# Optimization experiments

Hardware: AMD Instinct MI355X
Metric: run time of the kernel (lower is better)

The kernel has to match this reference:

```python
import jax, jax.numpy as jnp
import numpy as np

B, S, D = 4, 2048, 2048
H, HD = 16, 128
ROPE_THETA = 10000.0


def rotate_half(x):
    half = x.shape[-1] // 2
    return jnp.concatenate([-x[..., half:], x[..., :half]], axis=-1)


def setup_inputs() -> dict:
    key = jax.random.key(0)
    ks = jax.random.split(key, 5)
    scale = 1.0 / np.sqrt(D)
    x = jax.random.normal(ks[0], (B, S, D), dtype=jnp.float32)
    wq = jax.random.normal(ks[1], (D, H * HD), dtype=jnp.float32) * scale
    wk = jax.random.normal(ks[2], (D, H * HD), dtype=jnp.float32) * scale
    wv = jax.random.normal(ks[3], (D, H * HD), dtype=jnp.float32) * scale
    wo = jax.random.normal(ks[4], (H * HD, D), dtype=jnp.float32) * scale
    # RoPE frequencies: freqs_cis real/imag parts, shape [S, HD//2]
    inv_freq = 1.0 / (ROPE_THETA ** (np.arange(0, HD, 2, dtype=np.float32) / HD))
    t = np.arange(S, dtype=np.float32)
    freqs = np.outer(t, inv_freq)  # [S, HD//2]
    cos = jnp.asarray(np.cos(freqs), dtype=jnp.float32)
    sin = jnp.asarray(np.sin(freqs), dtype=jnp.float32)
    return {"x": x, "wq": wq, "wk": wk, "wv": wv, "wo": wo, "cos": cos, "sin": sin}


def reference(x, wq, wk, wv, wo, cos, sin):
    batch, seq_len, _ = x.shape
    # QKV projections (no bias), reshape to [b, h, s, d]
    q = (x @ wq).reshape(batch, seq_len, H, HD).transpose(0, 2, 1, 3)
    k = (x @ wk).reshape(batch, seq_len, H, HD).transpose(0, 2, 1, 3)
    v = (x @ wv).reshape(batch, seq_len, H, HD)  # [b, s, h, d]
    # RoPE (half-split / rotate_half convention)
    cos_full = jnp.concatenate([cos, cos], axis=-1)[None, None, :seq_len, :]
    sin_full = jnp.concatenate([sin, sin], axis=-1)[None, None, :seq_len, :]
    q = q * cos_full + rotate_half(q) * sin_full
    k = k * cos_full + rotate_half(k) * sin_full
    # Scaled dot-product attention with causal mask
    logits = jnp.einsum('bhqd,bhkd->bhqk', q, k) / jnp.sqrt(jnp.float32(HD))
    causal = jnp.tril(jnp.ones((seq_len, seq_len), dtype=bool))
    logits = jnp.where(causal[None, None, :, :], logits, -1e10)
    weights = jax.nn.softmax(logits, axis=-1)
    out = jnp.einsum('bhqk,bkhd->bqhd', weights, v)
    out = out.reshape(batch, seq_len, H * HD)
    return out @ wo
```

## Files before the change

kernel.cpp:

```cpp
#include <hip/hip_runtime.h>
#include <cstdint>
#include <cstddef>

typedef unsigned short u16;
using bf16x8  = __attribute__((ext_vector_type(8))) short;
using floatx4 = __attribute__((ext_vector_type(4))) float;

__device__ __forceinline__ u16 f2bf(float f) {
    union { float f; unsigned u; } v; v.f = f;
    unsigned r = v.u + 0x7fffu + ((v.u >> 16) & 1u);
    return (u16)(r >> 16);
}
__device__ __forceinline__ float bf2f(u16 h) {
    union { unsigned u; float f; } v; v.u = ((unsigned)h) << 16; return v.f;
}
__device__ __forceinline__ floatx4 mfma16(bf16x8 a, bf16x8 b, floatx4 c) {
    return __builtin_amdgcn_mfma_f32_16x16x32_bf16(a, b, c, 0, 0, 0);
}
using gptr_t = const __attribute__((address_space(1))) unsigned int*;
using lptr_t = __attribute__((address_space(3))) unsigned int*;
__device__ __forceinline__ void lds16(const void* g, void* l) {
    __builtin_amdgcn_global_load_lds((gptr_t)g, (lptr_t)l, 16, 0, 0);
}
typedef __attribute__((address_space(3))) const u16* lds_cp;
__device__ __forceinline__ bf16x8 dsr128(const u16* p) {
    bf16x8 r;
    asm volatile("ds_read_b128 %0, %1" : "=v"(r) : "v"((lds_cp)p));
    return r;
}

#define ATT_SCALE 0.1275758218522532f

__global__ __launch_bounds__(256) void prep(const float* __restrict__ x,
                                            const float* __restrict__ wq, const float* __restrict__ wk,
                                            const float* __restrict__ wv, const float* __restrict__ wo,
                                            u16* __restrict__ xb,
                                            u16* __restrict__ wqkvb, u16* __restrict__ wob) {
    const int z = blockIdx.z;
    const int tx = threadIdx.x, ty = threadIdx.y;
    if (z < 4) {
        __shared__ float t[64][65];
        const float* in = (z == 0) ? wq : (z == 1) ? wk : (z == 2) ? wv : wo;
        u16* out = (z < 3) ? (wqkvb + (size_t)z * 2048 * 2048) : wob;
        int k0 = blockIdx.x * 64, n0 = blockIdx.y * 64;
#pragma unroll
        for (int i = 0; i < 16; ++i) {
            int r = i * 4 + ty;
            t[r][tx] = in[(size_t)(k0 + r) * 2048 + n0 + tx];
        }
        __syncthreads();
#pragma unroll
        for (int i = 0; i < 16; ++i) {
            int r = i * 4 + ty;
            out[(size_t)(n0 + r) * 2048 + k0 + tx] = f2bf(t[tx][r]);
        }
    } else {
        const int flat = ty * 64 + tx;
        const size_t base = (size_t)(blockIdx.y * 32 + blockIdx.x) * 256 + flat;
        const size_t stride = 1024 * 256;
#pragma unroll
        for (int it = 0; it < 16; ++it) {
            size_t i = (base + it * stride) * 4;
            float4 v = *(const float4*)&x[i];
            ushort4 r; r.x = f2bf(v.x); r.y = f2bf(v.y); r.z = f2bf(v.z); r.w = f2bf(v.w);
            *(ushort4*)&xb[i] = r;
        }
    }
}

template <int MODE>
__global__ __launch_bounds__(512, 2) void gemm_bt(const u16* __restrict__ A, const u16* __restrict__ B,
                                                  u16* __restrict__ Qo, u16* __restrict__ Ko, u16* __restrict__ Vt,
                                                  float* __restrict__ Co,
                                                  const float* __restrict__ cosb, const float* __restrict__ sinb) {
    __shared__ __align__(16) u16 sA[2][16384];
    __shared__ __align__(16) u16 sB[2][16384];

    const int nbx = (MODE == 0) ? 24 : 8;
    const int bid = blockIdx.x;
    const int q8 = (int)gridDim.x >> 3;
    const int wg = (bid & 7) * q8 + (bid >> 3);
    const int bx = wg % nbx, by = wg / nbx;
    const int m0 = by << 8, n0 = bx << 8;

    const int tid = threadIdx.x;
    const int w = tid >> 6, lane = tid & 63;
    const int wm = w >> 2, wn = w & 3;
    const int m16 = lane & 15, q4 = lane >> 4;
    const int lr = lane >> 3;
    const int lc8 = (lane & 7) ^ lr;
    const int wnbase = (wn >> 1) * 128 + (wn & 1) * 32;

    const u16* Ag = A + (size_t)(m0 + w * 16 + lr) * 2048 + lc8 * 8;
    const u16* Bg = B + (size_t)(n0 + w * 16 + lr) * 2048 + lc8 * 8;

    const int swz0 = ((q4 ^ (m16 & 7)) << 3);
    const int swz1 = (((4 + q4) ^ (m16 & 7)) << 3);

    floatx4 acc[8][4];
#pragma unroll
    for (int r = 0; r < 8; ++r)
#pragma unroll
        for (int c = 0; c < 4; ++c) acc[r][c] = (floatx4)0.0f;
    bf16x8 af[4][2];
    bf16x8 bf[4][2];

#define STAGE_A(b, h, t) do { \
    lds16(Ag + (size_t)((h) * 128) * 2048 + (t) * 64,     &sA[b][(h) * 8192 + w * 1024]);       \
    lds16(Ag + (size_t)((h) * 128 + 8) * 2048 + (t) * 64, &sA[b][(h) * 8192 + w * 1024 + 512]); \
} while (0)
#define STAGE_B(b, h, t) do { \
    lds16(Bg + (size_t)((h) * 128) * 2048 + (t) * 64,     &sB[b][(h) * 8192 + w * 1024]);       \
    lds16(Bg + (size_t)((h) * 128 + 8) * 2048 + (t) * 64, &sB[b][(h) * 8192 + w * 1024 + 512]); \
} while (0)
#define BAR() __builtin_amdgcn_s_barrier()
#define WAITL0() do { asm volatile("s_waitcnt lgkmcnt(0)" ::: "memory"); __builtin_amdgcn_sched_barrier(0); } while (0)
#define WAITL8() asm volatile("s_waitcnt lgkmcnt(8)" ::: "memory")
#define LDA_(cur, mq) do { _Pragma("unroll") for (int fr = 0; fr < 4; ++fr) { \
    const u16* p = &sA[cur][(wm * 128 + (mq) * 64 + fr * 16 + m16) * 64];      \
    af[fr][0] = dsr128(&p[swz0]);                                              \
    af[fr][1] = dsr128(&p[swz1]); } } while (0)
#define LDB_(cur, nq) do { _Pragma("unroll") for (int c = 0; c < 2; ++c) {     \
    const int j = (nq) * 2 + c;                                                \
    const u16* p = &sB[cur][(wnbase + (j & 1) * 16 + (j >> 1) * 64 + m16) * 64]; \
    bf[j][0] = dsr128(&p[swz0]);                                               \
    bf[j][1] = dsr128(&p[swz1]); } } while (0)
#define MM_(mq, nq) do { _Pragma("unroll") for (int kk = 0; kk < 2; ++kk)      \
    _Pragma("unroll") for (int fr = 0; fr < 4; ++fr)                           \
    _Pragma("unroll") for (int c = 0; c < 2; ++c)                              \
        acc[(mq) * 4 + fr][(nq) * 2 + c] =                                     \
            mfma16(af[fr][kk], bf[(nq) * 2 + c][kk], acc[(mq) * 4 + fr][(nq) * 2 + c]); } while (0)

    const int NT = 32;

    STAGE_B(0, 0, 0); STAGE_B(0, 1, 0);
    STAGE_A(0, 0, 0); STAGE_A(0, 1, 0);
    STAGE_B(1, 0, 1); STAGE_B(1, 1, 1);
    asm volatile("s_waitcnt vmcnt(4)" ::: "memory");
    __builtin_amdgcn_s_barrier();

#pragma unroll 2
    for (int t = 0; t < NT; ++t) {
        const int cur = t & 1;
        LDB_(cur, 0);
        LDA_(cur, 0);
        if (t + 1 < NT) STAGE_A(cur ^ 1, 0, t + 1);
        WAITL8();
        BAR();
        WAITL0();
        __builtin_amdgcn_s_setprio(1); MM_(0, 0); __builtin_amdgcn_s_setprio(0);
        BAR();
        LDB_(cur, 1);
        if (t + 1 < NT) STAGE_A(cur ^ 1, 1, t + 1);
        BAR();
        WAITL0();
        __builtin_amdgcn_s_setprio(1); MM_(0, 1); __builtin_amdgcn_s_setprio(0);
        BAR();
        LDA_(cur, 1);
        if (t + 2 < NT) STAGE_B(cur, 0, t + 2);
        BAR();
        WAITL0();
        __builtin_amdgcn_s_setprio(1); MM_(1, 1); __builtin_amdgcn_s_setprio(0);
        BAR();
        if (t + 2 < NT) STAGE_B(cur, 1, t + 2);
        BAR();
        __builtin_amdgcn_s_setprio(1); MM_(1, 0); __builtin_amdgcn_s_setprio(0);
        if (t + 2 < NT)      { asm volatile("s_waitcnt vmcnt(4)" ::: "memory"); }
        else if (t + 1 < NT) { asm volatile("s_waitcnt vmcnt(0)" ::: "memory"); }
        BAR();
    }

#undef STAGE_A
#undef STAGE_B
#undef BAR
#undef WAITL0
#undef WAITL8
#undef LDA_
#undef LDB_
#undef MM_

    if (MODE == 0) {
        const int which = n0 >> 11;
        if (which < 2) {
            u16* dst = (which == 0) ? Qo : Ko;
            const float sc = (which == 0) ? ATT_SCALE : 1.0f;
            const int h = ((n0 >> 7) + (wn >> 1)) & 15;
            const int dp0 = (wn & 1) * 32 + m16;
#pragma unroll
            for (int fr = 0; fr < 8; ++fr) {
                const int mb = m0 + wm * 128 + fr * 16 + q4 * 4;
#pragma unroll
                for (int c0 = 0; c0 < 2; ++c0) {
                    const int dp = dp0 + c0 * 16;
#pragma unroll
                    for (int i = 0; i < 4; ++i) {
                        const int mm = mb + i;
                        const int b = mm >> 11, s = mm & 2047;
                        const float cs = cosb[(size_t)s * 64 + dp];
                        const float sn = sinb[(size_t)s * 64 + dp];
                        const float lo = acc[fr][c0][i], hi = acc[fr][c0 + 2][i];
                        const size_t base = ((size_t)((b * 16 + h) * 2048 + s) << 7) + dp;
                        dst[base]      = f2bf((lo * cs - hi * sn) * sc);
                        dst[base + 64] = f2bf((hi * cs + lo * sn) * sc);
                    }
                }
            }
        } else {
#pragma unroll
            for (int fr = 0; fr < 8; ++fr) {
                const int mb = m0 + wm * 128 + fr * 16 + q4 * 4;
                const int b = mb >> 11, s = mb & 2047;
#pragma unroll
                for (int c = 0; c < 4; ++c) {
                    const int n = n0 + wnbase + (c & 1) * 16 + (c >> 1) * 64 + m16;
                    const int h = (n >> 7) & 15, d = n & 127;
                    ushort4 pk;
                    pk.x = f2bf(acc[fr][c][0]); pk.y = f2bf(acc[fr][c][1]);
                    pk.z = f2bf(acc[fr][c][2]); pk.w = f2bf(acc[fr][c][3]);
                    *(ushort4*)&Vt[((size_t)((b * 16 + h) * 128 + d)) * 2048 + s] = pk;
                }
            }
        }
    } else {
#pragma unroll
        for (int fr = 0; fr < 8; ++fr) {
            const int mb = m0 + wm * 128 + fr * 16 + q4 * 4;
#pragma unroll
            for (int c = 0; c < 4; ++c) {
                const int n = n0 + wnbase + (c & 1) * 16 + (c >> 1) * 64 + m16;
#pragma unroll
                for (int i = 0; i < 4; ++i)
                    Co[(size_t)(mb + i) * 2048 + n] = acc[fr][c][i];
            }
        }
    }
}

__global__ __launch_bounds__(512) void attn_kernel(const u16* __restrict__ Q, const u16* __restrict__ K,
                                                   const u16* __restrict__ VT, u16* __restrict__ AO) {
    __shared__ __align__(16) u16 ks[64 * 128];
    __shared__ __align__(16) u16 vts[128 * 64];
    __shared__ __align__(16) u16 ps[256 * 64];
    static const int iqmap[8] = {7, 6, 5, 4, 0, 1, 2, 3};
    const int bx = blockIdx.x;
    const int iq = iqmap[bx >> 6];
    const int bh = bx & 63;
    const int b = bh >> 4, h = bh & 15;
    const u16* Qg = Q  + (size_t)bh * (2048 * 128);
    const u16* Kg = K  + (size_t)bh * (2048 * 128);
    const u16* Vg = VT + (size_t)bh * (128 * 2048);
    const int tid = threadIdx.x, w = tid >> 6, lane = tid & 63;
    const int m16 = lane & 15, q4 = lane >> 4;
    const int jn = 4 * iq + 4;
    const int key = m16 & 7;

    const int qrow = iq * 256 + w * 32;
    bf16x8 qf[2][4];
#pragma unroll
    for (int rm = 0; rm < 2; ++rm)
#pragma unroll
        for (int kk = 0; kk < 4; ++kk)
            qf[rm][kk] = *(const bf16x8*)&Qg[(size_t)(qrow + rm * 16 + m16) * 128 + kk * 32 + q4 * 8];

    floatx4 o[2][8];
#pragma unroll
    for (int rm = 0; rm < 2; ++rm)
#pragma unroll
        for (int c = 0; c < 8; ++c) o[rm][c] = (floatx4)0.0f;
    float mrow[2] = {-1e30f, -1e30f}, lrow[2] = {0.0f, 0.0f};

    const int kr0 = tid >> 4,          kc0 = tid & 15;
    const int kr1 = (512 + tid) >> 4,  kc1 = tid & 15;
    const int vr0 = tid >> 3,          vc0 = tid & 7;
    const int vr1 = (512 + tid) >> 3,  vc1 = tid & 7;
    uint4 kreg0, kreg1, vreg0, vreg1;

#define LOADKV(j) do { \
    kreg0 = *(const uint4*)&Kg[(size_t)((j) * 64 + kr0) * 128 + kc0 * 8]; \
    kreg1 = *(const uint4*)&Kg[(size_t)((j) * 64 + kr1) * 128 + kc1 * 8]; \
    vreg0 = *(const uint4*)&Vg[(size_t)vr0 * 2048 + (j) * 64 + vc0 * 8];  \
    vreg1 = *(const uint4*)&Vg[(size_t)vr1 * 2048 + (j) * 64 + vc1 * 8];  \
} while (0)

    LOADKV(0);

    for (int j = 0; j < jn; ++j) {
        asm volatile("" ::: "memory");
        __builtin_amdgcn_s_barrier();
        asm volatile("" ::: "memory");
        *(uint4*)&ks[kr0 * 128 + ((kc0 ^ (kr0 & 7)) * 8)] = kreg0;
        *(uint4*)&ks[kr1 * 128 + ((kc1 ^ (kr1 & 7)) * 8)] = kreg1;
        *(uint4*)&vts[vr0 * 64 + ((vc0 ^ (vr0 & 7)) * 8)] = vreg0;
        *(uint4*)&vts[vr1 * 64 + ((vc1 ^ (vr1 & 7)) * 8)] = vreg1;
        if (j + 1 < jn) LOADKV(j + 1);
        asm volatile("s_waitcnt lgkmcnt(0)" ::: "memory");
        __builtin_amdgcn_s_barrier();
        asm volatile("" ::: "memory");

        if (j * 64 > qrow + 31) continue;

        floatx4 sacc[2][4];
#pragma unroll
        for (int rm = 0; rm < 2; ++rm)
#pragma unroll
            for (int r = 0; r < 4; ++r) sacc[rm][r] = (floatx4)0.0f;
        __builtin_amdgcn_s_setprio(1);
#pragma unroll
        for (int kk = 0; kk < 4; ++kk) {
            bf16x8 kb[4];
#pragma unroll
            for (int r = 0; r < 4; ++r)
                kb[r] = *(const bf16x8*)&ks[(r * 16 + m16) * 128 + (((kk * 4 + q4) ^ key) * 8)];
#pragma unroll
            for (int rm = 0; rm < 2; ++rm)
#pragma unroll
                for (int r = 0; r < 4; ++r)
                    sacc[rm][r] = mfma16(kb[r], qf[rm][kk], sacc[rm][r]);
        }
        __builtin_amdgcn_s_setprio(0);

        if (j >= 4 * iq) {
#pragma unroll
            for (int rm = 0; rm < 2; ++rm) {
                const int qg = qrow + rm * 16 + m16;
#pragma unroll
                for (int r = 0; r < 4; ++r)
#pragma unroll
                    for (int i = 0; i < 4; ++i) {
                        int kg = j * 64 + r * 16 + q4 * 4 + i;
                        if (kg > qg) sacc[rm][r][i] = -1e30f;
                    }
            }
        }

#pragma unroll
        for (int rm = 0; rm < 2; ++rm) {
            float pmax = -1e30f;
#pragma unroll
            for (int r = 0; r < 4; ++r)
#pragma unroll
                for (int i = 0; i < 4; ++i) pmax = fmaxf(pmax, sacc[rm][r][i]);
            pmax = fmaxf(pmax, __shfl_xor(pmax, 16));
            pmax = fmaxf(pmax, __shfl_xor(pmax, 32));
            if (__any(pmax - mrow[rm] > 8.0f)) {
                float mnew = fmaxf(mrow[rm], pmax);
                float alpha = __builtin_amdgcn_exp2f(mrow[rm] - mnew);
                mrow[rm] = mnew;
                lrow[rm] *= alpha;
                float abc[4];
#pragma unroll
                for (int i = 0; i < 4; ++i) abc[i] = __shfl(alpha, q4 * 4 + i);
#pragma unroll
                for (int c = 0; c < 8; ++c)
#pragma unroll
                    for (int i = 0; i < 4; ++i) o[rm][c][i] *= abc[i];
            }

            float psum = 0.0f;
            const int prow = (w * 32 + rm * 16 + m16) * 64;
#pragma unroll
            for (int r = 0; r < 4; ++r) {
                float p0 = __builtin_amdgcn_exp2f(sacc[rm][r][0] - mrow[rm]);
                float p1 = __builtin_amdgcn_exp2f(sacc[rm][r][1] - mrow[rm]);
                float p2 = __builtin_amdgcn_exp2f(sacc[rm][r][2] - mrow[rm]);
                float p3 = __builtin_amdgcn_exp2f(sacc[rm][r][3] - mrow[rm]);
                psum += (p0 + p1) + (p2 + p3);
                ushort4 pk; pk.x = f2bf(p0); pk.y = f2bf(p1); pk.z = f2bf(p2); pk.w = f2bf(p3);
                *(ushort4*)&ps[prow + ((r * 16 + q4 * 4) ^ (key << 3))] = pk;
            }
            psum += __shfl_xor(psum, 16);
            psum += __shfl_xor(psum, 32);
            lrow[rm] += psum;
        }

#pragma unroll
        for (int kk = 0; kk < 2; ++kk) {
            bf16x8 pa[2];
#pragma unroll
            for (int rm = 0; rm < 2; ++rm)
                pa[rm] = *(const bf16x8*)&ps[(w * 32 + rm * 16 + m16) * 64 + ((kk * 32 + q4 * 8) ^ (key << 3))];
            __builtin_amdgcn_s_setprio(1);
#pragma unroll
            for (int ch = 0; ch < 2; ++ch) {
                bf16x8 vb[4];
#pragma unroll
                for (int c = 0; c < 4; ++c)
                    vb[c] = *(const bf16x8*)&vts[((ch * 4 + c) * 16 + m16) * 64 + (((kk * 4 + q4) ^ key) * 8)];
#pragma unroll
                for (int rm = 0; rm < 2; ++rm)
#pragma unroll
                    for (int c = 0; c < 4; ++c)
                        o[rm][ch * 4 + c] = mfma16(pa[rm], vb[c], o[rm][ch * 4 + c]);
            }
            __builtin_amdgcn_s_setprio(0);
        }
    }
#undef LOADKV

#pragma unroll
    for (int rm = 0; rm < 2; ++rm) {
        float linv = __builtin_amdgcn_rcpf(lrow[rm]);
        float li[4];
#pragma unroll
        for (int i = 0; i < 4; ++i) li[i] = __shfl(linv, q4 * 4 + i);
#pragma unroll
        for (int c = 0; c < 8; ++c)
#pragma unroll
            for (int i = 0; i < 4; ++i) {
                int s = qrow + rm * 16 + q4 * 4 + i;
                int d = c * 16 + m16;
                AO[((size_t)(b * 2048 + s)) * 2048 + h * 128 + d] = f2bf(o[rm][c][i] * li[i]);
            }
    }
}

extern "C" void kernel_launch(void* const* d_in, const int* in_sizes, int n_in,
                              void* d_out, int out_size, void* d_ws, size_t ws_size,
                              hipStream_t stream) {
    const float* x    = (const float*)d_in[0];
    const float* wq   = (const float*)d_in[1];
    const float* wk   = (const float*)d_in[2];
    const float* wv   = (const float*)d_in[3];
    const float* wo   = (const float*)d_in[4];
    const float* cosb = (const float*)d_in[5];
    const float* sinb = (const float*)d_in[6];
    float* out = (float*)d_out;

    char* ws = (char*)d_ws;
    u16* xb    = (u16*)(ws);
    u16* AO    = xb;
    u16* wqkvb = (u16*)(ws + 33554432);
    u16* wob   = (u16*)(ws + 58720256);
    u16* Qb    = (u16*)(ws + 67108864);
    u16* Kb    = (u16*)(ws + 100663296);
    u16* Vtb   = (u16*)(ws + 134217728);

    prep<<<dim3(32, 32, 5), dim3(64, 4), 0, stream>>>(x, wq, wk, wv, wo, xb, wqkvb, wob);

    gemm_bt<0><<<768, 512, 0, stream>>>(xb, wqkvb, Qb, Kb, Vtb, nullptr, cosb, sinb);
    attn_kernel<<<512, 512, 0, stream>>>(Qb, Kb, Vtb, AO);
    gemm_bt<1><<<256, 512, 0, stream>>>(AO, wob, nullptr, nullptr, nullptr, out, nullptr, nullptr);
}
```

Measured before the change: 537.0 us.

## Keep attention P tile in registers via cross-lane shuffles instead of LDS

```diff
diff --git a/kernel.cpp b/kernel.cpp
--- a/kernel.cpp
+++ b/kernel.cpp
@@ -26,6 +26,11 @@
 __device__ __forceinline__ bf16x8 dsr128(const u16* p) {
     bf16x8 r;
     asm volatile("ds_read_b128 %0, %1" : "=v"(r) : "v"((lds_cp)p));
+    return r;
+}
+__device__ __forceinline__ unsigned cvt_pk_bf16(float lo, float hi) {
+    unsigned r;
+    asm("v_cvt_pk_bf16_f32 %0, %1, %2" : "=v"(r) : "v"(lo), "v"(hi));
     return r;
 }
 
@@ -236,11 +241,10 @@
     }
 }
 
-__global__ __launch_bounds__(512) void attn_kernel(const u16* __restrict__ Q, const u16* __restrict__ K,
-                                                   const u16* __restrict__ VT, u16* __restrict__ AO) {
+__global__ __launch_bounds__(512, 4) void attn_kernel(const u16* __restrict__ Q, const u16* __restrict__ K,
+                                                      const u16* __restrict__ VT, u16* __restrict__ AO) {
     __shared__ __align__(16) u16 ks[64 * 128];
     __shared__ __align__(16) u16 vts[128 * 64];
-    __shared__ __align__(16) u16 ps[256 * 64];
     static const int iqmap[8] = {7, 6, 5, 4, 0, 1, 2, 3};
     const int bx = blockIdx.x;
     const int iq = iqmap[bx >> 6];
@@ -333,13 +337,14 @@
             }
         }
 
+        bf16x8 paf[2][2];
 #pragma unroll
         for (int rm = 0; rm < 2; ++rm) {
-            float pmax = -1e30f;
-#pragma unroll
-            for (int r = 0; r < 4; ++r)
-#pragma unroll
-                for (int i = 0; i < 4; ++i) pmax = fmaxf(pmax, sacc[rm][r][i]);
+            float t0 = fmaxf(fmaxf(sacc[rm][0][0], sacc[rm][0][1]), fmaxf(sacc[rm][0][2], sacc[rm][0][3]));
+            float t1 = fmaxf(fmaxf(sacc[rm][1][0], sacc[rm][1][1]), fmaxf(sacc[rm][1][2], sacc[rm][1][3]));
+            float t2 = fmaxf(fmaxf(sacc[rm][2][0], sacc[rm][2][1]), fmaxf(sacc[rm][2][2], sacc[rm][2][3]));
+            float t3 = fmaxf(fmaxf(sacc[rm][3][0], sacc[rm][3][1]), fmaxf(sacc[rm][3][2], sacc[rm][3][3]));
+            float pmax = fmaxf(fmaxf(t0, t1), fmaxf(t2, t3));
             pmax = fmaxf(pmax, __shfl_xor(pmax, 16));
             pmax = fmaxf(pmax, __shfl_xor(pmax, 32));
             if (__any(pmax - mrow[rm] > 8.0f)) {
@@ -356,8 +361,8 @@
                     for (int i = 0; i < 4; ++i) o[rm][c][i] *= abc[i];
             }
 
+            unsigned wv[4][2];
             float psum = 0.0f;
-            const int prow = (w * 32 + rm * 16 + m16) * 64;
 #pragma unroll
             for (int r = 0; r < 4; ++r) {
                 float p0 = __builtin_amdgcn_exp2f(sacc[rm][r][0] - mrow[rm]);
@@ -365,20 +370,47 @@
                 float p2 = __builtin_amdgcn_exp2f(sacc[rm][r][2] - mrow[rm]);
                 float p3 = __builtin_amdgcn_exp2f(sacc[rm][r][3] - mrow[rm]);
                 psum += (p0 + p1) + (p2 + p3);
-                ushort4 pk; pk.x = f2bf(p0); pk.y = f2bf(p1); pk.z = f2bf(p2); pk.w = f2bf(p3);
-                *(ushort4*)&ps[prow + ((r * 16 + q4 * 4) ^ (key << 3))] = pk;
+                wv[r][0] = cvt_pk_bf16(p0, p1);
+                wv[r][1] = cvt_pk_bf16(p2, p3);
             }
             psum += __shfl_xor(psum, 16);
             psum += __shfl_xor(psum, 32);
             lrow[rm] += psum;
+
+            const bool lowq = (q4 < 2);
+            unsigned a0 = lowq ? wv[0][0] : wv[1][0];
+            unsigned a1 = lowq ? wv[0][1] : wv[1][1];
+            unsigned a2 = lowq ? wv[2][0] : wv[3][0];
+            unsigned a3 = lowq ? wv[2][1] : wv[3][1];
+            unsigned s0 = lowq ? wv[1][0] : wv[0][0];
+            unsigned s1 = lowq ? wv[1][1] : wv[0][1];
+            unsigned s2 = lowq ? wv[3][0] : wv[2][0];
+            unsigned s3 = lowq ? wv[3][1] : wv[2][1];
+            unsigned g0 = (unsigned)__shfl_xor((int)s0, 32);
+            unsigned g1 = (unsigned)__shfl_xor((int)s1, 32);
+            unsigned g2 = (unsigned)__shfl_xor((int)s2, 32);
+            unsigned g3 = (unsigned)__shfl_xor((int)s3, 32);
+            const bool sendA = (((q4 ^ (q4 >> 1)) & 1) != 0);
+            unsigned u0 = sendA ? a0 : g0, k0_ = sendA ? g0 : a0;
+            unsigned u1 = sendA ? a1 : g1, k1_ = sendA ? g1 : a1;
+            unsigned u2 = sendA ? a2 : g2, k2_ = sendA ? g2 : a2;
+            unsigned u3 = sendA ? a3 : g3, k3_ = sendA ? g3 : a3;
+            unsigned r0 = (unsigned)__shfl_xor((int)u0, 16);
+            unsigned r1 = (unsigned)__shfl_xor((int)u1, 16);
+            unsigned r2 = (unsigned)__shfl_xor((int)u2, 16);
+            unsigned r3 = (unsigned)__shfl_xor((int)u3, 16);
+            const bool keptLow = ((q4 & 1) == 0);
+            union { unsigned u[4]; bf16x8 v; } pz;
+            pz.u[0] = keptLow ? k0_ : r0;  pz.u[1] = keptLow ? k1_ : r1;
+            pz.u[2] = keptLow ? r0 : k0_;  pz.u[3] = keptLow ? r1 : k1_;
+            paf[rm][0] = pz.v;
+            pz.u[0] = keptLow ? k2_ : r2;  pz.u[1] = keptLow ? k3_ : r3;
+            pz.u[2] = keptLow ? r2 : k2_;  pz.u[3] = keptLow ? r3 : k3_;
+            paf[rm][1] = pz.v;
         }
 
 #pragma unroll
         for (int kk = 0; kk < 2; ++kk) {
-            bf16x8 pa[2];
-#pragma unroll
-            for (int rm = 0; rm < 2; ++rm)
-                pa[rm] = *(const bf16x8*)&ps[(w * 32 + rm * 16 + m16) * 64 + ((kk * 32 + q4 * 8) ^ (key << 3))];
             __builtin_amdgcn_s_setprio(1);
 #pragma unroll
             for (int ch = 0; ch < 2; ++ch) {
@@ -390,7 +422,7 @@
                 for (int rm = 0; rm < 2; ++rm)
 #pragma unroll
                     for (int c = 0; c < 4; ++c)
-                        o[rm][ch * 4 + c] = mfma16(pa[rm], vb[c], o[rm][ch * 4 + c]);
+                        o[rm][ch * 4 + c] = mfma16(paf[rm][kk], vb[c], o[rm][ch * 4 + c]);
             }
             __builtin_amdgcn_s_setprio(0);
         }
```

New measurement: 754.0 us. +40.4%, slower.
